# Optimization experiments

Measured on AMD Instinct MI355X. Metric: run time of the kernel, lower is better.

## Reference

```python
import jax, jax.numpy as jnp
import numpy as np

HIDDEN = 2048
INTER = 5632
TOKENS = 8192


def setup_inputs() -> dict:
    key = jax.random.key(0)
    k1, k2, k3 = jax.random.split(key, 3)
    x = jax.random.normal(k1, (TOKENS, HIDDEN), dtype=jnp.float32)
    # gate_up_weight = [gate_weight | up_weight], shape [hidden, 2*intermediate]
    gate_up_weight = jax.random.normal(k2, (HIDDEN, 2 * INTER), dtype=jnp.float32) * (1.0 / np.sqrt(HIDDEN))
    down_weight = jax.random.normal(k3, (INTER, HIDDEN), dtype=jnp.float32) * (1.0 / np.sqrt(INTER))
    return {"x": x, "gate_up_weight": gate_up_weight, "down_weight": down_weight}


def reference(x, gate_up_weight, down_weight):
    # Fused SwiGLU expert MLP: SiLU(x @ Wg) * (x @ Wu) @ Wd
    inter = gate_up_weight.shape[1] // 2
    gate_up = jnp.matmul(x, gate_up_weight)          # [T, 2*I]
    gate, up = gate_up[:, :inter], gate_up[:, inter:]
    hidden = jax.nn.silu(gate) * up                   # [T, I]
    out = jnp.matmul(hidden, down_weight)             # [T, H]
    return out.astype(x.dtype)
```

## Files before the change

kernel.cpp:

```cpp
#include <hip/hip_runtime.h>
#include <stdint.h>

typedef unsigned short u16;
typedef __attribute__((ext_vector_type(8))) __bf16 bf16x8;
typedef __attribute__((ext_vector_type(8))) u16 u16x8;
typedef __attribute__((ext_vector_type(4))) float f32x4;

#define HID 2048
#define INTER 5632
#define TOKENS 8192

__device__ __forceinline__ u16 f2bf(float f) {
  uint32_t u = __builtin_bit_cast(uint32_t, f);
  u += 0x7fffu + ((u >> 16) & 1u);
  return (u16)(u >> 16);
}

__device__ __forceinline__ void gld_lds16(const u16* g, u16* l) {
  __builtin_amdgcn_global_load_lds(
      (const __attribute__((address_space(1))) unsigned int*)g,
      (__attribute__((address_space(3))) unsigned int*)l, 16, 0, 0);
}


__global__ void k_cvt_x(const float* __restrict__ in, u16* __restrict__ out) {
  size_t i = (size_t)blockIdx.x * 256 + threadIdx.x;
  const float4* p = (const float4*)(in + i * 8);
  float4 a = p[0], b = p[1];
  u16x8 o;
  o[0] = f2bf(a.x); o[1] = f2bf(a.y); o[2] = f2bf(a.z); o[3] = f2bf(a.w);
  o[4] = f2bf(b.x); o[5] = f2bf(b.y); o[6] = f2bf(b.z); o[7] = f2bf(b.w);
  *(u16x8*)(out + i * 8) = o;
}

__global__ void k_transpose(const float* __restrict__ in, u16* __restrict__ out,
                            int R, int C) {
  __shared__ float t[32][33];
  int c0 = blockIdx.x * 32, r0 = blockIdx.y * 32;
  int tx = threadIdx.x, ty = threadIdx.y;
#pragma unroll
  for (int r = 0; r < 4; ++r) {
    int i = ty + r * 8;
    t[i][tx] = in[(size_t)(r0 + i) * C + c0 + tx];
  }
  __syncthreads();
#pragma unroll
  for (int r = 0; r < 4; ++r) {
    int i = ty + r * 8;
    out[(size_t)(c0 + i) * R + r0 + tx] = f2bf(t[tx][i]);
  }
}


#define STAGE(dst, srcBase, stride, kt)                                        \
  do {                                                                         \
    const int _k0 = (kt) * 64;                                                 \
    _Pragma("unroll") for (int _r = 0; _r < 2; ++_r) {                         \
      const int _prow = _r * 64 + wid * 8 + srow;                              \
      const u16* _src = (srcBase) + (size_t)_prow * (stride) + _k0 +           \
                        ((schunk ^ (_prow & 7)) * 8);                          \
      gld_lds16(_src, (dst) + _prow * 64 + schunk * 8);                        \
    }                                                                          \
  } while (0)

#define LOAD_A(bufp, mh)                                                       \
  do {                                                                         \
    _Pragma("unroll") for (int _jj = 0; _jj < 4; ++_jj) {                      \
      const int _row = ((mh)*4 + _jj) * 32 + wm * 16 + cb;                     \
      _Pragma("unroll") for (int _ks = 0; _ks < 2; ++_ks) {                    \
        const int _ch = (_ks * 4 + hi) ^ (cb & 7);                             \
        aF[_jj][_ks] = *(const bf16x8*)((bufp) + _row * 64 + _ch * 8);         \
      }                                                                        \
    }                                                                          \
  } while (0)

#define LOAD_B(bufp, nh)                                                       \
  do {                                                                         \
    _Pragma("unroll") for (int _nn = 0; _nn < 2; ++_nn) {                      \
      const int _row = ((nh)*2 + _nn) * 64 + wn * 16 + cb;                     \
      _Pragma("unroll") for (int _ks = 0; _ks < 2; ++_ks) {                    \
        const int _ch = (_ks * 4 + hi) ^ (cb & 7);                             \
        bF[_nn][_ks] = *(const bf16x8*)((bufp) + _row * 64 + _ch * 8);         \
      }                                                                        \
    }                                                                          \
  } while (0)

#define MMA_Q(mh, nh)                                                          \
  do {                                                                         \
    _Pragma("unroll") for (int _ks = 0; _ks < 2; ++_ks)                        \
    _Pragma("unroll") for (int _jj = 0; _jj < 4; ++_jj)                        \
    _Pragma("unroll") for (int _nn = 0; _nn < 2; ++_nn)                        \
      acc[(mh)*4 + _jj][(nh)*2 + _nn] =                                        \
          __builtin_amdgcn_mfma_f32_16x16x32_bf16(                             \
              aF[_jj][_ks], bF[_nn][_ks], acc[(mh)*4 + _jj][(nh)*2 + _nn],     \
              0, 0, 0);                                                        \
  } while (0)

#define KTILE_BODY(bufA, bufB, nA, nB, gA0, gB0, gA1, gB1, STRIDE, hn, tn)     \
  do {                                                                         \
                                                            \
    if (hn) STAGE(nA, gA0, STRIDE, tn);                                        \
    LOAD_A(bufA, 0); LOAD_B(bufB, 0);                                          \
    __builtin_amdgcn_s_barrier();                                              \
    __builtin_amdgcn_s_setprio(1); MMA_Q(0, 0); __builtin_amdgcn_s_setprio(0); \
    __builtin_amdgcn_s_barrier();                                              \
                                                            \
    if (hn) STAGE(nB, gB0, STRIDE, tn);                                        \
    LOAD_A(bufA, 1);                                                           \
    __builtin_amdgcn_s_barrier();                                              \
    __builtin_amdgcn_s_setprio(1); MMA_Q(1, 0); __builtin_amdgcn_s_setprio(0); \
    __builtin_amdgcn_sched_barrier(0);                                         \
    if (hn) asm volatile("s_waitcnt vmcnt(4)" ::: "memory");                   \
    else    asm volatile("s_waitcnt vmcnt(0)" ::: "memory");                   \
    __builtin_amdgcn_s_barrier();                                              \
                                                            \
    if (hn) STAGE((nA) + 128 * 64, gA1, STRIDE, tn);                           \
    LOAD_B(bufB, 1);                                                           \
    __builtin_amdgcn_s_barrier();                                              \
    __builtin_amdgcn_s_setprio(1); MMA_Q(1, 1); __builtin_amdgcn_s_setprio(0); \
    __builtin_amdgcn_s_barrier();                                              \
                                                            \
    if (hn) STAGE((nB) + 128 * 64, gB1, STRIDE, tn);                           \
    LOAD_A(bufA, 0);                                                           \
    __builtin_amdgcn_s_barrier();                                              \
    __builtin_amdgcn_s_setprio(1); MMA_Q(0, 1); __builtin_amdgcn_s_setprio(0); \
    __builtin_amdgcn_sched_barrier(0);                                         \
    if (hn) asm volatile("s_waitcnt vmcnt(2)" ::: "memory");                   \
    __builtin_amdgcn_s_barrier();                                              \
  } while (0)

__global__ __launch_bounds__(512, 2) void k_gemm1_8ph(
    const u16* __restrict__ xb, const u16* __restrict__ w1t,
    u16* __restrict__ hid) {
  __shared__ __align__(16) u16 sA[2][256 * 64];
  __shared__ __align__(16) u16 sB[2][256 * 64];
  const int NT = HID / 64;
  const int o = blockIdx.x;
  const int swz = (o & 7) * 176 + (o >> 3);
  const int brow = (swz / 44) * 256, bcol = (swz % 44) * 128;

  const int tid = threadIdx.x, lane = tid & 63, wid = tid >> 6;
  const int wm = wid >> 2, wn = wid & 3;
  const int cb = lane & 15, hi = lane >> 4;
  const int srow = lane >> 3, schunk = lane & 7;

  f32x4 acc[8][4] = {};
  bf16x8 aF[4][2], bF[2][2];

  const u16* gA0 = xb + (size_t)brow * HID;
  const u16* gA1 = gA0 + (size_t)128 * HID;
  const u16* gB0 = w1t + (size_t)bcol * HID;
  const u16* gB1 = w1t + (size_t)(INTER + bcol) * HID;

  STAGE(sA[0], gA0, HID, 0);
  STAGE(sB[0], gB0, HID, 0);
  STAGE(sA[0] + 128 * 64, gA1, HID, 0);
  STAGE(sB[0] + 128 * 64, gB1, HID, 0);
  asm volatile("s_waitcnt vmcnt(2)" ::: "memory");
  __builtin_amdgcn_s_barrier();

  for (int t = 0; t < NT; ++t) {
    u16* bufA = sA[t & 1];
    u16* bufB = sB[t & 1];
    u16* nA = sA[(t & 1) ^ 1];
    u16* nB = sB[(t & 1) ^ 1];
    const bool hn = (t + 1 < NT);
    KTILE_BODY(bufA, bufB, nA, nB, gA0, gB0, gA1, gB1, HID, hn, t + 1);
  }

#pragma unroll
  for (int j = 0; j < 8; ++j)
#pragma unroll
    for (int nn = 0; nn < 2; ++nn) {
      const int col = bcol + nn * 64 + wn * 16 + cb;
#pragma unroll
      for (int i = 0; i < 4; ++i) {
        const int row = brow + j * 32 + wm * 16 + hi * 4 + i;
        float g = acc[j][nn][i], u = acc[j][nn + 2][i];
        float h = g / (1.0f + __expf(-g)) * u;
        hid[(size_t)row * INTER + col] = f2bf(h);
      }
    }
}

__global__ __launch_bounds__(512, 2) void k_gemm2_8ph(
    const u16* __restrict__ hid, const u16* __restrict__ w2t,
    float* __restrict__ out) {
  __shared__ __align__(16) u16 sA[2][256 * 64];
  __shared__ __align__(16) u16 sB[2][256 * 64];
  const int NT = INTER / 64;
  const int o = blockIdx.x;
  const int swz = (o & 7) * 32 + (o >> 3);
  const int brow = (swz / 8) * 256, bcol = (swz % 8) * 256;

  const int tid = threadIdx.x, lane = tid & 63, wid = tid >> 6;
  const int wm = wid >> 2, wn = wid & 3;
  const int cb = lane & 15, hi = lane >> 4;
  const int srow = lane >> 3, schunk = lane & 7;

  f32x4 acc[8][4] = {};
  bf16x8 aF[4][2], bF[2][2];

  const u16* gA0 = hid + (size_t)brow * INTER;
  const u16* gA1 = gA0 + (size_t)128 * INTER;
  const u16* gB0 = w2t + (size_t)bcol * INTER;
  const u16* gB1 = w2t + (size_t)(bcol + 128) * INTER;

  STAGE(sA[0], gA0, INTER, 0);
  STAGE(sB[0], gB0, INTER, 0);
  STAGE(sA[0] + 128 * 64, gA1, INTER, 0);
  STAGE(sB[0] + 128 * 64, gB1, INTER, 0);
  asm volatile("s_waitcnt vmcnt(2)" ::: "memory");
  __builtin_amdgcn_s_barrier();

  for (int t = 0; t < NT; ++t) {
    u16* bufA = sA[t & 1];
    u16* bufB = sB[t & 1];
    u16* nA = sA[(t & 1) ^ 1];
    u16* nB = sB[(t & 1) ^ 1];
    const bool hn = (t + 1 < NT);
    KTILE_BODY(bufA, bufB, nA, nB, gA0, gB0, gA1, gB1, INTER, hn, t + 1);
  }

#pragma unroll
  for (int j = 0; j < 8; ++j)
#pragma unroll
    for (int n = 0; n < 4; ++n) {
      const int col = bcol + n * 64 + wn * 16 + cb;
#pragma unroll
      for (int i = 0; i < 4; ++i) {
        const int row = brow + j * 32 + wm * 16 + hi * 4 + i;
        out[(size_t)row * HID + col] = acc[j][n][i];
      }
    }
}


extern "C" void kernel_launch(void* const* d_in, const int* in_sizes, int n_in,
                              void* d_out, int out_size, void* d_ws, size_t ws_size,
                              hipStream_t stream) {
  const float* x  = (const float*)d_in[0];
  const float* w1 = (const float*)d_in[1];
  const float* w2 = (const float*)d_in[2];
  float* out = (float*)d_out;

  const size_t off_xb  = 0;
  const size_t off_w1t = 33554432;
  const size_t off_w2t = off_w1t + 46137344;
  const size_t off_hid = off_w2t + 23068672;
  const size_t need    = off_hid + 92274688;
  if (ws_size < need) return;

  char* ws = (char*)d_ws;
  u16* xb  = (u16*)(ws + off_xb);
  u16* w1t = (u16*)(ws + off_w1t);
  u16* w2t = (u16*)(ws + off_w2t);
  u16* hid = (u16*)(ws + off_hid);

  k_cvt_x<<<TOKENS * HID / 8 / 256, 256, 0, stream>>>(x, xb);
  dim3 tb(32, 8);
  k_transpose<<<dim3((2 * INTER) / 32, HID / 32), tb, 0, stream>>>(w1, w1t, HID, 2 * INTER);
  k_transpose<<<dim3(HID / 32, INTER / 32), tb, 0, stream>>>(w2, w2t, INTER, HID);

  k_gemm1_8ph<<<(TOKENS / 256) * (INTER / 128), 512, 0, stream>>>(xb, w1t, hid);
  k_gemm2_8ph<<<(TOKENS / 256) * (HID / 256), 512, 0, stream>>>(hid, w2t, out);
}
```

Measured before the change: 1.001 ms.

## Issue prefetch stages earlier in GEMM pipeline and widen weight transpose tiles

The weight transpose moves to 64x64 tiles with float4 loads and 16-byte bf16 stores, which cuts the number of narrow global transactions during weight preparation. Inside the GEMM k-loop, the A0 and B0 stages of the next tile are now issued together at the start, and the remaining stages move one phase earlier, with vmcnt waits adjusted to match. This gives global-to-LDS loads more time to land before they are consumed. The cost is more outstanding loads per wave, and the hand-tuned wait counts must stay consistent with the new issue order.

```diff
diff --git a/kernel.cpp b/kernel.cpp
--- a/kernel.cpp
+++ b/kernel.cpp
@@ -33,21 +33,28 @@
   *(u16x8*)(out + i * 8) = o;
 }
 
-__global__ void k_transpose(const float* __restrict__ in, u16* __restrict__ out,
-                            int R, int C) {
-  __shared__ float t[32][33];
-  int c0 = blockIdx.x * 32, r0 = blockIdx.y * 32;
-  int tx = threadIdx.x, ty = threadIdx.y;
+__global__ __launch_bounds__(256) void k_transpose64(
+    const float* __restrict__ in, u16* __restrict__ out, int R, int C) {
+  __shared__ float t[64][65];
+  int c0 = blockIdx.x * 64, r0 = blockIdx.y * 64;
+  int tid = threadIdx.x;
+  int tx = tid & 15, ry = tid >> 4;
 #pragma unroll
   for (int r = 0; r < 4; ++r) {
-    int i = ty + r * 8;
-    t[i][tx] = in[(size_t)(r0 + i) * C + c0 + tx];
+    int row = r * 16 + ry;
+    float4 v = *(const float4*)(in + (size_t)(r0 + row) * C + c0 + tx * 4);
+    t[row][tx * 4 + 0] = v.x; t[row][tx * 4 + 1] = v.y;
+    t[row][tx * 4 + 2] = v.z; t[row][tx * 4 + 3] = v.w;
   }
   __syncthreads();
-#pragma unroll
-  for (int r = 0; r < 4; ++r) {
-    int i = ty + r * 8;
-    out[(size_t)(c0 + i) * R + r0 + tx] = f2bf(t[tx][i]);
+  int cc = tid >> 2, seg = tid & 3;
+#pragma unroll
+  for (int h = 0; h < 2; ++h) {
+    int rr0 = seg * 16 + h * 8;
+    u16x8 o;
+#pragma unroll
+    for (int j = 0; j < 8; ++j) o[j] = f2bf(t[rr0 + j][cc]);
+    *(u16x8*)(out + (size_t)(c0 + cc) * R + r0 + rr0) = o;
   }
 }
 
@@ -99,33 +106,35 @@
 #define KTILE_BODY(bufA, bufB, nA, nB, gA0, gB0, gA1, gB1, STRIDE, hn, tn)     \
   do {                                                                         \
                                                             \
-    if (hn) STAGE(nA, gA0, STRIDE, tn);                                        \
+    if (hn) { STAGE(nA, gA0, STRIDE, tn); STAGE(nB, gB0, STRIDE, tn); }        \
     LOAD_A(bufA, 0); LOAD_B(bufB, 0);                                          \
     __builtin_amdgcn_s_barrier();                                              \
     __builtin_amdgcn_s_setprio(1); MMA_Q(0, 0); __builtin_amdgcn_s_setprio(0); \
-    __builtin_amdgcn_s_barrier();                                              \
-                                                            \
-    if (hn) STAGE(nB, gB0, STRIDE, tn);                                        \
+    __builtin_amdgcn_sched_barrier(0);                                         \
+    if (hn) asm volatile("s_waitcnt vmcnt(6)" ::: "memory");                   \
+    else    asm volatile("s_waitcnt vmcnt(2)" ::: "memory");                   \
+    __builtin_amdgcn_s_barrier();                                              \
+                                                            \
+    if (hn) STAGE((nA) + 128 * 64, gA1, STRIDE, tn);                           \
     LOAD_A(bufA, 1);                                                           \
     __builtin_amdgcn_s_barrier();                                              \
     __builtin_amdgcn_s_setprio(1); MMA_Q(1, 0); __builtin_amdgcn_s_setprio(0); \
     __builtin_amdgcn_sched_barrier(0);                                         \
-    if (hn) asm volatile("s_waitcnt vmcnt(4)" ::: "memory");                   \
+    if (hn) asm volatile("s_waitcnt vmcnt(6)" ::: "memory");                   \
     else    asm volatile("s_waitcnt vmcnt(0)" ::: "memory");                   \
     __builtin_amdgcn_s_barrier();                                              \
                                                             \
-    if (hn) STAGE((nA) + 128 * 64, gA1, STRIDE, tn);                           \
+    if (hn) STAGE((nB) + 128 * 64, gB1, STRIDE, tn);                           \
     LOAD_B(bufB, 1);                                                           \
     __builtin_amdgcn_s_barrier();                                              \
     __builtin_amdgcn_s_setprio(1); MMA_Q(1, 1); __builtin_amdgcn_s_setprio(0); \
     __builtin_amdgcn_s_barrier();                                              \
                                                             \
-    if (hn) STAGE((nB) + 128 * 64, gB1, STRIDE, tn);                           \
     LOAD_A(bufA, 0);                                                           \
     __builtin_amdgcn_s_barrier();                                              \
     __builtin_amdgcn_s_setprio(1); MMA_Q(0, 1); __builtin_amdgcn_s_setprio(0); \
     __builtin_amdgcn_sched_barrier(0);                                         \
-    if (hn) asm volatile("s_waitcnt vmcnt(2)" ::: "memory");                   \
+    if (hn) asm volatile("s_waitcnt vmcnt(4)" ::: "memory");                   \
     __builtin_amdgcn_s_barrier();                                              \
   } while (0)
 
@@ -156,7 +165,8 @@
   STAGE(sB[0], gB0, HID, 0);
   STAGE(sA[0] + 128 * 64, gA1, HID, 0);
   STAGE(sB[0] + 128 * 64, gB1, HID, 0);
-  asm volatile("s_waitcnt vmcnt(2)" ::: "memory");
+  __builtin_amdgcn_sched_barrier(0);
+  asm volatile("s_waitcnt vmcnt(4)" ::: "memory");
   __builtin_amdgcn_s_barrier();
 
   for (int t = 0; t < NT; ++t) {
@@ -210,7 +220,8 @@
   STAGE(sB[0], gB0, INTER, 0);
   STAGE(sA[0] + 128 * 64, gA1, INTER, 0);
   STAGE(sB[0] + 128 * 64, gB1, INTER, 0);
-  asm volatile("s_waitcnt vmcnt(2)" ::: "memory");
+  __builtin_amdgcn_sched_barrier(0);
+  asm volatile("s_waitcnt vmcnt(4)" ::: "memory");
   __builtin_amdgcn_s_barrier();
 
   for (int t = 0; t < NT; ++t) {
@@ -258,9 +269,8 @@
   u16* hid = (u16*)(ws + off_hid);
 
   k_cvt_x<<<TOKENS * HID / 8 / 256, 256, 0, stream>>>(x, xb);
-  dim3 tb(32, 8);
-  k_transpose<<<dim3((2 * INTER) / 32, HID / 32), tb, 0, stream>>>(w1, w1t, HID, 2 * INTER);
-  k_transpose<<<dim3(HID / 32, INTER / 32), tb, 0, stream>>>(w2, w2t, INTER, HID);
+  k_transpose64<<<dim3((2 * INTER) / 64, HID / 64), 256, 0, stream>>>(w1, w1t, HID, 2 * INTER);
+  k_transpose64<<<dim3(HID / 64, INTER / 64), 256, 0, stream>>>(w2, w2t, INTER, HID);
 
   k_gemm1_8ph<<<(TOKENS / 256) * (INTER / 128), 512, 0, stream>>>(xb, w1t, hid);
   k_gemm2_8ph<<<(TOKENS / 256) * (HID / 256), 512, 0, stream>>>(hid, w2t, out);
```

Result: faster. 866.9 us (-13.4%).
